# Kernel tuning notes

Measured on AMD Instinct MI355X. Metric: run time of the kernel, lower is better.

The kernel has to match this reference:

```python
import jax, jax.numpy as jnp
import numpy as np

TAU0 = 0.5  # Concrete temperature (init kwarg tau0)
EPS = float(np.finfo(np.float32).eps)  # torch.finfo(float32).eps clamp


def _linear_params(key, fan_in, fan_out):
    # matches torch nn.Linear default init: U(-1/sqrt(fan_in), 1/sqrt(fan_in))
    bound = 1.0 / np.sqrt(fan_in)
    kw, kb = jax.random.split(key)
    W = jax.random.uniform(kw, (fan_in, fan_out), minval=-bound, maxval=bound, dtype=jnp.float32)
    b = jax.random.uniform(kb, (fan_out,), minval=-bound, maxval=bound, dtype=jnp.float32)
    return W, b


def setup_inputs() -> dict:
    key = jax.random.key(0)
    ks = jax.random.split(key, 6)
    B, D, K = 32768, 200, 10
    w1, b1 = _linear_params(ks[0], D, 100)    # dense1
    w2, b2 = _linear_params(ks[1], 100, 100)  # dense2
    wl, bl = _linear_params(ks[2], 100, D)    # logits
    wo, bo = _linear_params(ks[3], D, 2)      # output (requires D == 200)
    x = jax.random.normal(ks[4], (B, D), dtype=jnp.float32)
    uniform = jax.random.uniform(ks[5], (B, K, D), dtype=jnp.float32)
    return {"x": x, "uniform": uniform,
            "w1": w1, "b1": b1, "w2": w2, "b2": b2,
            "wl": wl, "bl": bl, "wo": wo, "bo": bo}


def reference(x, uniform, w1, b1, w2, b2, wl, bl, wo, bo):
    # selector MLP
    h = jax.nn.relu(x @ w1 + b1)            # (B, 100)
    h = jax.nn.relu(h @ w2 + b2)            # (B, 100)
    logits = h @ wl + bl                    # (B, D)
    # SampleConcrete (training path): gumbel-softmax over features, max over k samples
    u = jnp.clip(uniform, EPS, 1.0)         # (B, K, D)
    gumbel = -jnp.log(-jnp.log(u))
    noisy = (gumbel + logits[:, None, :]) / TAU0
    samples = jax.nn.softmax(noisy, axis=-1).max(axis=1)  # (B, D); repeat_count == 1
    xs = x * samples
    preds = jax.nn.softmax(xs @ wo + bo, axis=-1)          # (B, 2)
    # hsic(xs, preds) in the original is computed but discarded -> omitted
    return preds, samples
```

## Files before the change

### kernel.cpp

```cpp
#include <hip/hip_runtime.h>
#include <hip/hip_bf16.h>

template <int K, int N, int NP, bool RELU>
__launch_bounds__(256)
__global__ void mlp_gemm(const float* __restrict__ A, const float* __restrict__ W,
                         const float* __restrict__ bias, float* __restrict__ C) {
  constexpr int BM = 64;
  constexpr int KC = 20;
  constexpr int TM = 8;
  constexpr int TN = NP / 32;
  constexpr int BMP = BM + 4;

  __shared__ float At[KC * BMP];
  __shared__ float Ws[KC * NP];

  const int t = threadIdx.x;
  const int tx = t & 31;
  const int ty = t >> 5;
  const int rowBase = blockIdx.x * BM;

  float acc[TM][TN];
#pragma unroll
  for (int i = 0; i < TM; i++)
#pragma unroll
    for (int j = 0; j < TN; j++) acc[i][j] = 0.0f;

  for (int kc = 0; kc < K; kc += KC) {
#pragma unroll
    for (int i = t; i < BM * KC; i += 256) {
      int r = i / KC;
      int k = i - r * KC;
      At[k * BMP + r] = A[(rowBase + r) * K + kc + k];
    }
#pragma unroll
    for (int i = t; i < KC * NP; i += 256) {
      int k = i / NP;
      int c = i - k * NP;
      Ws[i] = (c < N) ? W[(kc + k) * N + c] : 0.0f;
    }
    __syncthreads();

#pragma unroll
    for (int k = 0; k < KC; k++) {
      float a[TM], b[TN];
      *(float4*)&a[0] = *(const float4*)&At[k * BMP + ty * TM];
      *(float4*)&a[4] = *(const float4*)&At[k * BMP + ty * TM + 4];
#pragma unroll
      for (int j = 0; j < TN; j += 4)
        *(float4*)&b[j] = *(const float4*)&Ws[k * NP + tx * TN + j];
#pragma unroll
      for (int i = 0; i < TM; i++)
#pragma unroll
        for (int j = 0; j < TN; j++) acc[i][j] += a[i] * b[j];
    }
    __syncthreads();
  }

  const int c0 = tx * TN;
  if (c0 < N) {
#pragma unroll
    for (int i = 0; i < TM; i++) {
      const int r = rowBase + ty * TM + i;
#pragma unroll
      for (int j = 0; j < TN; j += 4) {
        float4 v;
        v.x = acc[i][j + 0] + bias[c0 + j + 0];
        v.y = acc[i][j + 1] + bias[c0 + j + 1];
        v.z = acc[i][j + 2] + bias[c0 + j + 2];
        v.w = acc[i][j + 3] + bias[c0 + j + 3];
        if (RELU) {
          v.x = fmaxf(v.x, 0.0f);
          v.y = fmaxf(v.y, 0.0f);
          v.z = fmaxf(v.z, 0.0f);
          v.w = fmaxf(v.w, 0.0f);
        }
        *(float4*)&C[r * N + c0 + j] = v;
      }
    }
  }
}

__launch_bounds__(256)
__global__ void concrete_kernel(const float* __restrict__ x,
                                const float* __restrict__ uniform,
                                const float* __restrict__ logits,
                                const float* __restrict__ wo,
                                const float* __restrict__ bo,
                                float* __restrict__ out, int B) {
  const int lane = threadIdx.x & 63;
  const int wave = threadIdx.x >> 6;
  const int b = blockIdx.x * 4 + wave;
  if (b >= B) return;

  constexpr float EPS = 1.1920929e-07f;
  constexpr int D = 200;

  float lg[4], xv[4], smax[4];
#pragma unroll
  for (int i = 0; i < 4; i++) {
    const int d = lane + 64 * i;
    const bool v = (d < D);
    lg[i] = v ? logits[b * D + d] : 0.0f;
    xv[i] = v ? x[b * D + d] : 0.0f;
    smax[i] = 0.0f;
  }

  const float* __restrict__ urow = uniform + (size_t)b * 10 * D;
#pragma unroll 1
  for (int k = 0; k < 10; k++) {
    const float* __restrict__ u = urow + k * D;
    float noisy[4];
    float mloc = -1e30f;
#pragma unroll
    for (int i = 0; i < 4; i++) {
      const int d = lane + 64 * i;
      if (d < D) {
        float uu = u[d];
        uu = fminf(fmaxf(uu, EPS), 1.0f);
        const float g = -__logf(-__logf(uu));
        noisy[i] = (g + lg[i]) * 2.0f;
        mloc = fmaxf(mloc, noisy[i]);
      } else {
        noisy[i] = -1e30f;
      }
    }
#pragma unroll
    for (int off = 32; off > 0; off >>= 1)
      mloc = fmaxf(mloc, __shfl_xor(mloc, off, 64));

    float e[4];
    float ssum = 0.0f;
#pragma unroll
    for (int i = 0; i < 4; i++) {
      e[i] = (lane + 64 * i < D) ? __expf(noisy[i] - mloc) : 0.0f;
      ssum += e[i];
    }
#pragma unroll
    for (int off = 32; off > 0; off >>= 1)
      ssum += __shfl_xor(ssum, off, 64);

    const float inv = 1.0f / ssum;
#pragma unroll
    for (int i = 0; i < 4; i++) smax[i] = fmaxf(smax[i], e[i] * inv);
  }

  float p0 = 0.0f, p1 = 0.0f;
  const int samplesBase = B * 2;
#pragma unroll
  for (int i = 0; i < 4; i++) {
    const int d = lane + 64 * i;
    if (d < D) {
      const float s = smax[i];
      out[samplesBase + b * D + d] = s;
      const float xs = xv[i] * s;
      p0 += xs * wo[d * 2 + 0];
      p1 += xs * wo[d * 2 + 1];
    }
  }
#pragma unroll
  for (int off = 32; off > 0; off >>= 1) {
    p0 += __shfl_xor(p0, off, 64);
    p1 += __shfl_xor(p1, off, 64);
  }
  if (lane == 0) {
    const float z0 = p0 + bo[0];
    const float z1 = p1 + bo[1];
    const float m = fmaxf(z0, z1);
    const float e0 = __expf(z0 - m);
    const float e1 = __expf(z1 - m);
    const float s = e0 + e1;
    out[b * 2 + 0] = e0 / s;
    out[b * 2 + 1] = e1 / s;
  }
}

extern "C" void kernel_launch(void* const* d_in, const int* in_sizes, int n_in,
                              void* d_out, int out_size, void* d_ws, size_t ws_size,
                              hipStream_t stream) {
  const float* x  = (const float*)d_in[0];
  const float* un = (const float*)d_in[1];
  const float* w1 = (const float*)d_in[2];
  const float* b1 = (const float*)d_in[3];
  const float* w2 = (const float*)d_in[4];
  const float* b2 = (const float*)d_in[5];
  const float* wl = (const float*)d_in[6];
  const float* bl = (const float*)d_in[7];
  const float* wo = (const float*)d_in[8];
  const float* bo = (const float*)d_in[9];
  float* out = (float*)d_out;

  const int B = in_sizes[0] / 200;

  float* h2 = (float*)d_ws;
  float* h1 = h2 + (size_t)B * 100;
  float* logits = h1;

  mlp_gemm<200, 100, 128, true><<<B / 64, 256, 0, stream>>>(x, w1, b1, h1);
  mlp_gemm<100, 100, 128, true><<<B / 64, 256, 0, stream>>>(h1, w2, b2, h2);
  mlp_gemm<100, 200, 256, false><<<B / 64, 256, 0, stream>>>(h2, wl, bl, logits);
  concrete_kernel<<<B / 4, 256, 0, stream>>>(x, un, logits, wo, bo, out, B);
}
```

Baseline: 573.0 us.

## Fuse MLP layers 1-2 and logits GEMM with concrete sampling kernel

Merges the first two MLP GEMMs into one kernel that keeps h1 in shared memory, and fuses the logits GEMM with the Gumbel-softmax concrete kernel so logits stay in LDS. Four launches become two, removing the global-memory round trips for h1 and logits. The concrete stage also preloads all 10 uniform rows per batch row into registers, so loads can be in flight together. The cost is heavy LDS use (about 57KB in the second kernel) and higher register pressure, which may limit occupancy.

New measurement: 566.2 us. About the same (-1.2%).

```diff
diff --git a/kernel.cpp b/kernel.cpp
--- a/kernel.cpp
+++ b/kernel.cpp
@@ -1,176 +1,265 @@
 #include <hip/hip_runtime.h>
 #include <hip/hip_bf16.h>
 
-template <int K, int N, int NP, bool RELU>
 __launch_bounds__(256)
-__global__ void mlp_gemm(const float* __restrict__ A, const float* __restrict__ W,
-                         const float* __restrict__ bias, float* __restrict__ C) {
-  constexpr int BM = 64;
-  constexpr int KC = 20;
-  constexpr int TM = 8;
-  constexpr int TN = NP / 32;
-  constexpr int BMP = BM + 4;
-
+__global__ void fused_mlp12(const float* __restrict__ x,
+                            const float* __restrict__ w1, const float* __restrict__ b1,
+                            const float* __restrict__ w2, const float* __restrict__ b2,
+                            float* __restrict__ h2out) {
+  constexpr int BM = 64, KC = 20, BMP = 68;
   __shared__ float At[KC * BMP];
-  __shared__ float Ws[KC * NP];
+  __shared__ float Ws[KC * 128];
+  __shared__ float h1T[100 * BMP];
 
   const int t = threadIdx.x;
   const int tx = t & 31;
   const int ty = t >> 5;
   const int rowBase = blockIdx.x * BM;
 
-  float acc[TM][TN];
-#pragma unroll
-  for (int i = 0; i < TM; i++)
-#pragma unroll
-    for (int j = 0; j < TN; j++) acc[i][j] = 0.0f;
-
-  for (int kc = 0; kc < K; kc += KC) {
+  float acc[8][4];
+#pragma unroll
+  for (int i = 0; i < 8; i++)
+#pragma unroll
+    for (int j = 0; j < 4; j++) acc[i][j] = 0.0f;
+
+  for (int kc = 0; kc < 200; kc += KC) {
 #pragma unroll
     for (int i = t; i < BM * KC; i += 256) {
-      int r = i / KC;
-      int k = i - r * KC;
-      At[k * BMP + r] = A[(rowBase + r) * K + kc + k];
-    }
-#pragma unroll
-    for (int i = t; i < KC * NP; i += 256) {
-      int k = i / NP;
-      int c = i - k * NP;
-      Ws[i] = (c < N) ? W[(kc + k) * N + c] : 0.0f;
-    }
-    __syncthreads();
-
+      int r = i / KC, k = i - r * KC;
+      At[k * BMP + r] = x[(rowBase + r) * 200 + kc + k];
+    }
+#pragma unroll
+    for (int i = t; i < KC * 128; i += 256) {
+      int k = i >> 7, c = i & 127;
+      Ws[i] = (c < 100) ? w1[(kc + k) * 100 + c] : 0.0f;
+    }
+    __syncthreads();
 #pragma unroll
     for (int k = 0; k < KC; k++) {
-      float a[TM], b[TN];
-      *(float4*)&a[0] = *(const float4*)&At[k * BMP + ty * TM];
-      *(float4*)&a[4] = *(const float4*)&At[k * BMP + ty * TM + 4];
-#pragma unroll
-      for (int j = 0; j < TN; j += 4)
-        *(float4*)&b[j] = *(const float4*)&Ws[k * NP + tx * TN + j];
-#pragma unroll
-      for (int i = 0; i < TM; i++)
-#pragma unroll
-        for (int j = 0; j < TN; j++) acc[i][j] += a[i] * b[j];
-    }
-    __syncthreads();
-  }
-
-  const int c0 = tx * TN;
-  if (c0 < N) {
-#pragma unroll
-    for (int i = 0; i < TM; i++) {
-      const int r = rowBase + ty * TM + i;
-#pragma unroll
-      for (int j = 0; j < TN; j += 4) {
-        float4 v;
-        v.x = acc[i][j + 0] + bias[c0 + j + 0];
-        v.y = acc[i][j + 1] + bias[c0 + j + 1];
-        v.z = acc[i][j + 2] + bias[c0 + j + 2];
-        v.w = acc[i][j + 3] + bias[c0 + j + 3];
-        if (RELU) {
-          v.x = fmaxf(v.x, 0.0f);
-          v.y = fmaxf(v.y, 0.0f);
-          v.z = fmaxf(v.z, 0.0f);
-          v.w = fmaxf(v.w, 0.0f);
-        }
-        *(float4*)&C[r * N + c0 + j] = v;
-      }
+      float a[8], b[4];
+      *(float4*)&a[0] = *(const float4*)&At[k * BMP + ty * 8];
+      *(float4*)&a[4] = *(const float4*)&At[k * BMP + ty * 8 + 4];
+      *(float4*)&b[0] = *(const float4*)&Ws[k * 128 + tx * 4];
+#pragma unroll
+      for (int i = 0; i < 8; i++)
+#pragma unroll
+        for (int j = 0; j < 4; j++) acc[i][j] += a[i] * b[j];
+    }
+    __syncthreads();
+  }
+
+  if (tx < 25) {
+#pragma unroll
+    for (int i = 0; i < 8; i++) {
+      const int r = ty * 8 + i;
+#pragma unroll
+      for (int j = 0; j < 4; j++) {
+        const int c = tx * 4 + j;
+        h1T[c * BMP + r] = fmaxf(acc[i][j] + b1[c], 0.0f);
+      }
+    }
+  }
+  __syncthreads();
+
+#pragma unroll
+  for (int i = 0; i < 8; i++)
+#pragma unroll
+    for (int j = 0; j < 4; j++) acc[i][j] = 0.0f;
+
+  for (int kc = 0; kc < 100; kc += KC) {
+#pragma unroll
+    for (int i = t; i < KC * 128; i += 256) {
+      int k = i >> 7, c = i & 127;
+      Ws[i] = (c < 100) ? w2[(kc + k) * 100 + c] : 0.0f;
+    }
+    __syncthreads();
+#pragma unroll
+    for (int k = 0; k < KC; k++) {
+      float a[8], b[4];
+      *(float4*)&a[0] = *(const float4*)&h1T[(kc + k) * BMP + ty * 8];
+      *(float4*)&a[4] = *(const float4*)&h1T[(kc + k) * BMP + ty * 8 + 4];
+      *(float4*)&b[0] = *(const float4*)&Ws[k * 128 + tx * 4];
+#pragma unroll
+      for (int i = 0; i < 8; i++)
+#pragma unroll
+        for (int j = 0; j < 4; j++) acc[i][j] += a[i] * b[j];
+    }
+    __syncthreads();
+  }
+
+  if (tx < 25) {
+#pragma unroll
+    for (int i = 0; i < 8; i++) {
+      const int r = rowBase + ty * 8 + i;
+      float4 v;
+      v.x = fmaxf(acc[i][0] + b2[tx * 4 + 0], 0.0f);
+      v.y = fmaxf(acc[i][1] + b2[tx * 4 + 1], 0.0f);
+      v.z = fmaxf(acc[i][2] + b2[tx * 4 + 2], 0.0f);
+      v.w = fmaxf(acc[i][3] + b2[tx * 4 + 3], 0.0f);
+      *(float4*)&h2out[r * 100 + tx * 4] = v;
     }
   }
 }
 
-__launch_bounds__(256)
-__global__ void concrete_kernel(const float* __restrict__ x,
-                                const float* __restrict__ uniform,
-                                const float* __restrict__ logits,
-                                const float* __restrict__ wo,
-                                const float* __restrict__ bo,
-                                float* __restrict__ out, int B) {
-  const int lane = threadIdx.x & 63;
-  const int wave = threadIdx.x >> 6;
-  const int b = blockIdx.x * 4 + wave;
-  if (b >= B) return;
-
+__launch_bounds__(512, 4)
+__global__ void fused_logits_concrete(const float* __restrict__ x,
+                                      const float* __restrict__ uniform,
+                                      const float* __restrict__ h2,
+                                      const float* __restrict__ wl, const float* __restrict__ bl,
+                                      const float* __restrict__ wo, const float* __restrict__ bo,
+                                      float* __restrict__ out, int B) {
+  constexpr int BM = 64, KC = 20, BMP = 68;
   constexpr float EPS = 1.1920929e-07f;
-  constexpr int D = 200;
-
-  float lg[4], xv[4], smax[4];
-#pragma unroll
-  for (int i = 0; i < 4; i++) {
-    const int d = lane + 64 * i;
-    const bool v = (d < D);
-    lg[i] = v ? logits[b * D + d] : 0.0f;
-    xv[i] = v ? x[b * D + d] : 0.0f;
-    smax[i] = 0.0f;
-  }
-
-  const float* __restrict__ urow = uniform + (size_t)b * 10 * D;
+  __shared__ float At[KC * BMP];
+  __shared__ float Ws[KC * 256];
+  __shared__ float lg[BM * 200];
+
+  const int t = threadIdx.x;
+  const int rowBase = blockIdx.x * BM;
+
+  {
+    const int tx = t & 31;
+    const int ty = t >> 5;
+    float acc[4][8];
+#pragma unroll
+    for (int i = 0; i < 4; i++)
+#pragma unroll
+      for (int j = 0; j < 8; j++) acc[i][j] = 0.0f;
+
+    for (int kc = 0; kc < 100; kc += KC) {
+      for (int i = t; i < BM * KC; i += 512) {
+        int r = i / KC, k = i - r * KC;
+        At[k * BMP + r] = h2[(rowBase + r) * 100 + kc + k];
+      }
+#pragma unroll
+      for (int i = t; i < KC * 256; i += 512) {
+        int k = i >> 8, c = i & 255;
+        Ws[i] = (c < 200) ? wl[(kc + k) * 200 + c] : 0.0f;
+      }
+      __syncthreads();
+#pragma unroll
+      for (int k = 0; k < KC; k++) {
+        float a[4], b[8];
+        *(float4*)&a[0] = *(const float4*)&At[k * BMP + ty * 4];
+        *(float4*)&b[0] = *(const float4*)&Ws[k * 256 + tx * 8];
+        *(float4*)&b[4] = *(const float4*)&Ws[k * 256 + tx * 8 + 4];
+#pragma unroll
+        for (int i = 0; i < 4; i++)
+#pragma unroll
+          for (int j = 0; j < 8; j++) acc[i][j] += a[i] * b[j];
+      }
+      __syncthreads();
+    }
+
+    if (tx < 25) {
+#pragma unroll
+      for (int i = 0; i < 4; i++) {
+        const int r = ty * 4 + i;
+        float4 v0, v1;
+        v0.x = acc[i][0] + bl[tx * 8 + 0];
+        v0.y = acc[i][1] + bl[tx * 8 + 1];
+        v0.z = acc[i][2] + bl[tx * 8 + 2];
+        v0.w = acc[i][3] + bl[tx * 8 + 3];
+        v1.x = acc[i][4] + bl[tx * 8 + 4];
+        v1.y = acc[i][5] + bl[tx * 8 + 5];
+        v1.z = acc[i][6] + bl[tx * 8 + 6];
+        v1.w = acc[i][7] + bl[tx * 8 + 7];
+        *(float4*)&lg[r * 200 + tx * 8] = v0;
+        *(float4*)&lg[r * 200 + tx * 8 + 4] = v1;
+      }
+    }
+    __syncthreads();
+  }
+
+  const int lane = t & 63;
+  const int wave = t >> 6;
+  const int samplesBase = B * 2;
+
 #pragma unroll 1
-  for (int k = 0; k < 10; k++) {
-    const float* __restrict__ u = urow + k * D;
-    float noisy[4];
-    float mloc = -1e30f;
+  for (int rr = 0; rr < 8; rr++) {
+    const int r = wave * 8 + rr;
+    const int b = rowBase + r;
+
+    float lgv[4], xv[4], smax[4];
 #pragma unroll
     for (int i = 0; i < 4; i++) {
       const int d = lane + 64 * i;
-      if (d < D) {
-        float uu = u[d];
-        uu = fminf(fmaxf(uu, EPS), 1.0f);
-        const float g = -__logf(-__logf(uu));
-        noisy[i] = (g + lg[i]) * 2.0f;
-        mloc = fmaxf(mloc, noisy[i]);
-      } else {
-        noisy[i] = -1e30f;
-      }
-    }
-#pragma unroll
-    for (int off = 32; off > 0; off >>= 1)
-      mloc = fmaxf(mloc, __shfl_xor(mloc, off, 64));
-
-    float e[4];
-    float ssum = 0.0f;
+      const bool v = (d < 200);
+      lgv[i] = v ? lg[r * 200 + d] : 0.0f;
+      xv[i] = v ? x[(size_t)b * 200 + d] : 0.0f;
+      smax[i] = 0.0f;
+    }
+
+    const float* __restrict__ u = uniform + (size_t)b * 2000;
+    float uu[10][4];
+#pragma unroll
+    for (int k = 0; k < 10; k++)
+#pragma unroll
+      for (int i = 0; i < 4; i++) {
+        const int d = lane + 64 * i;
+        uu[k][i] = (d < 200) ? u[k * 200 + d] : 0.5f;
+      }
+
+#pragma unroll
+    for (int k = 0; k < 10; k++) {
+      float noisy[4];
+      float mloc = -1e30f;
+#pragma unroll
+      for (int i = 0; i < 4; i++) {
+        if (lane + 64 * i < 200) {
+          float uc = fminf(fmaxf(uu[k][i], EPS), 1.0f);
+          const float g = -__logf(-__logf(uc));
+          noisy[i] = (g + lgv[i]) * 2.0f;
+          mloc = fmaxf(mloc, noisy[i]);
+        } else {
+          noisy[i] = -1e30f;
+        }
+      }
+#pragma unroll
+      for (int off = 32; off > 0; off >>= 1)
+        mloc = fmaxf(mloc, __shfl_xor(mloc, off, 64));
+
+      float e[4], ssum = 0.0f;
+#pragma unroll
+      for (int i = 0; i < 4; i++) {
+        e[i] = (lane + 64 * i < 200) ? __expf(noisy[i] - mloc) : 0.0f;
+        ssum += e[i];
+      }
+#pragma unroll
+      for (int off = 32; off > 0; off >>= 1)
+        ssum += __shfl_xor(ssum, off, 64);
+
+      const float inv = 1.0f / ssum;
+#pragma unroll
+      for (int i = 0; i < 4; i++) smax[i] = fmaxf(smax[i], e[i] * inv);
+    }
+
+    float p0 = 0.0f, p1 = 0.0f;
 #pragma unroll
     for (int i = 0; i < 4; i++) {
-      e[i] = (lane + 64 * i < D) ? __expf(noisy[i] - mloc) : 0.0f;
-      ssum += e[i];
-    }
-#pragma unroll
-    for (int off = 32; off > 0; off >>= 1)
-      ssum += __shfl_xor(ssum, off, 64);
-
-    const float inv = 1.0f / ssum;
-#pragma unroll
-    for (int i = 0; i < 4; i++) smax[i] = fmaxf(smax[i], e[i] * inv);
-  }
-
-  float p0 = 0.0f, p1 = 0.0f;
-  const int samplesBase = B * 2;
-#pragma unroll
-  for (int i = 0; i < 4; i++) {
-    const int d = lane + 64 * i;
-    if (d < D) {
-      const float s = smax[i];
-      out[samplesBase + b * D + d] = s;
-      const float xs = xv[i] * s;
-      p0 += xs * wo[d * 2 + 0];
-      p1 += xs * wo[d * 2 + 1];
-    }
-  }
-#pragma unroll
-  for (int off = 32; off > 0; off >>= 1) {
-    p0 += __shfl_xor(p0, off, 64);
-    p1 += __shfl_xor(p1, off, 64);
-  }
-  if (lane == 0) {
-    const float z0 = p0 + bo[0];
-    const float z1 = p1 + bo[1];
-    const float m = fmaxf(z0, z1);
-    const float e0 = __expf(z0 - m);
-    const float e1 = __expf(z1 - m);
-    const float s = e0 + e1;
-    out[b * 2 + 0] = e0 / s;
-    out[b * 2 + 1] = e1 / s;
+      const int d = lane + 64 * i;
+      if (d < 200) {
+        const float s = smax[i];
+        out[samplesBase + (size_t)b * 200 + d] = s;
+        const float xs = xv[i] * s;
+        p0 += xs * wo[d * 2 + 0];
+        p1 += xs * wo[d * 2 + 1];
+      }
+    }
+#pragma unroll
+    for (int off = 32; off > 0; off >>= 1) {
+      p0 += __shfl_xor(p0, off, 64);
+      p1 += __shfl_xor(p1, off, 64);
+    }
+    if (lane == 0) {
+      const float z0 = p0 + bo[0];
+      const float z1 = p1 + bo[1];
+      const float m = fmaxf(z0, z1);
+      const float e0 = __expf(z0 - m);
+      const float e1 = __expf(z1 - m);
+      out[b * 2 + 0] = e0 / (e0 + e1);
+      out[b * 2 + 1] = e1 / (e0 + e1);
+    }
   }
 }
 
@@ -190,13 +279,8 @@
   float* out = (float*)d_out;
 
   const int B = in_sizes[0] / 200;
-
   float* h2 = (float*)d_ws;
-  float* h1 = h2 + (size_t)B * 100;
-  float* logits = h1;
-
-  mlp_gemm<200, 100, 128, true><<<B / 64, 256, 0, stream>>>(x, w1, b1, h1);
-  mlp_gemm<100, 100, 128, true><<<B / 64, 256, 0, stream>>>(h1, w2, b2, h2);
-  mlp_gemm<100, 200, 256, false><<<B / 64, 256, 0, stream>>>(h2, wl, bl, logits);
-  concrete_kernel<<<B / 4, 256, 0, stream>>>(x, un, logits, wo, bo, out, B);
+
+  fused_mlp12<<<B / 64, 256, 0, stream>>>(x, w1, b1, w2, b2, h2);
+  fused_logits_concrete<<<B / 64, 512, 0, stream>>>(x, un, h2, wl, bl, wo, bo, out, B);
 }
```
